# Kernel optimization log

Measured on AMD Instinct MI355X. Metric: run time of the kernel, lower is better.

## Reference

```python
import jax, jax.numpy as jnp
import numpy as np

N_HEADS = 16
ROPE_BASE = 10000.0

def apply_rope(x):
    # x: [B, H, S, D] with D even; interleaved-pair RoPE (torchtune style)
    B, H, S, D = x.shape
    half = D // 2
    inv_freq = 1.0 / (ROPE_BASE ** (jnp.arange(0, half, dtype=jnp.float32) / half))
    angles = jnp.arange(S, dtype=jnp.float32)[:, None] * inv_freq[None, :]  # [S, D/2]
    cos = jnp.cos(angles)[None, None]  # [1,1,S,D/2]
    sin = jnp.sin(angles)[None, None]
    x1 = x[..., 0::2]
    x2 = x[..., 1::2]
    r1 = x1 * cos - x2 * sin
    r2 = x1 * sin + x2 * cos
    return jnp.stack([r1, r2], axis=-1).reshape(B, H, S, D)

def setup_inputs() -> dict:
    key = jax.random.key(0)
    ks = jax.random.split(key, 5)
    B, S, E = 2, 2048, 1024
    d_attn = 1024
    scale = 1.0 / np.sqrt(E)
    x = jax.random.normal(ks[0], (B, S, E), dtype=jnp.float32)
    Wq = jax.random.normal(ks[1], (d_attn, E), dtype=jnp.float32) * scale
    Wk = jax.random.normal(ks[2], (d_attn, E), dtype=jnp.float32) * scale
    Wv = jax.random.normal(ks[3], (d_attn, E), dtype=jnp.float32) * scale
    Wo = jax.random.normal(ks[4], (E, d_attn), dtype=jnp.float32) * scale
    return {"x": x, "Wq": Wq, "Wk": Wk, "Wv": Wv, "Wo": Wo}

def reference(x, Wq, Wk, Wv, Wo):
    B, S, E = x.shape
    d_attn = Wq.shape[0]
    hd = d_attn // N_HEADS
    attn_scale = 1.0 / np.sqrt(d_attn)
    # projections (nn.Linear: x @ W.T), split heads -> [B, H, S, hd]
    q = (x @ Wq.T).reshape(B, S, N_HEADS, hd).transpose(0, 2, 1, 3)
    k = (x @ Wk.T).reshape(B, S, N_HEADS, hd).transpose(0, 2, 1, 3)
    v = (x @ Wv.T).reshape(B, S, N_HEADS, hd).transpose(0, 2, 1, 3)
    q = apply_rope(q)
    k = apply_rope(k)
    scores = jnp.einsum('bhqd,bhkd->bhqk', q, k) * attn_scale  # [B,H,S,S]
    causal = jnp.tril(jnp.ones((S, S), dtype=bool))
    scores = jnp.where(causal[None, None], scores, -jnp.inf)
    probs = jax.nn.softmax(scores, axis=-1)  # dropout is identity in eval
    out = jnp.einsum('bhqk,bhkd->bhqd', probs, v)
    out = out.transpose(0, 2, 1, 3).reshape(B, S, d_attn)
    return out @ Wo.T
```

## Files before the change

kernel.cpp:

```cpp
#include <hip/hip_runtime.h>


typedef float  f32x4  __attribute__((ext_vector_type(4)));
typedef short  short8 __attribute__((ext_vector_type(8)));

#define MFMA16(a,b,c) __builtin_amdgcn_mfma_f32_16x16x32_bf16((a),(b),(c),0,0,0)
#define GLD_LDS16(g, l)                                                        \
  __builtin_amdgcn_global_load_lds(                                            \
      (const __attribute__((address_space(1))) unsigned int*)(g),              \
      (__attribute__((address_space(3))) unsigned int*)(l), 16, 0, 0)

__device__ __forceinline__ unsigned short f2bf(float f) {
  unsigned int x = __float_as_uint(f);
  x += 0x7fffu + ((x >> 16) & 1u);
  return (unsigned short)(x >> 16);
}
__device__ __forceinline__ float bf2f(unsigned short u) {
  return __uint_as_float(((unsigned int)u) << 16);
}
__device__ __forceinline__ unsigned int cvtpk_bf16(float lo, float hi) {
  unsigned int r;
  asm("v_cvt_pk_bf16_f32 %0, %1, %2" : "=v"(r) : "v"(lo), "v"(hi));
  return r;
}

__global__ __launch_bounds__(256) void cvt_all(const float* __restrict__ x,
                                               const float* __restrict__ wq,
                                               const float* __restrict__ wk,
                                               const float* __restrict__ wv,
                                               const float* __restrict__ wo,
                                               ushort* __restrict__ dst) {
  const int i = blockIdx.x * 256 + threadIdx.x;
  const float* src;
  int off;
  if (i < 1048576) { src = x; off = i; }
  else {
    const int j = i - 1048576;
    const int wsel = j >> 18;
    off = j & 262143;
    src = (wsel == 0) ? wq : (wsel == 1) ? wk : (wsel == 2) ? wv : wo;
  }
  const float4 v = ((const float4*)src)[off];
  ushort4 o = make_ushort4(f2bf(v.x), f2bf(v.y), f2bf(v.z), f2bf(v.w));
  ((ushort4*)dst)[i] = o;
}

template<int MODE, int BN, int BM>
__global__ __launch_bounds__(256) void gemm_bt(const ushort* __restrict__ A,
                                               const ushort* __restrict__ B,
                                               void* __restrict__ Cv,
                                               int K) {
  constexpr int NI = BN / 32;
  constexpr int MI = BM / 32;
  constexpr int AI = BM / 64;
  constexpr int BI = BN / 64;
  __shared__ __align__(16) short As0[BM * 32];
  __shared__ __align__(16) short As1[BM * 32];
  __shared__ __align__(16) short Bs0[BN * 32];
  __shared__ __align__(16) short Bs1[BN * 32];
  const int tid  = threadIdx.x;
  const int lane = tid & 63, w = tid >> 6;
  const int ln   = lane & 15, quad = lane >> 4;
  const int wm   = w >> 1, wn = w & 1;
  const int m0 = blockIdx.y * BM, n0 = blockIdx.x * BN;

  const int srow = lane >> 2;
  const int schk = (lane & 3) * 8;
  const int arow = w * (16 * AI);
  const int brow = w * (16 * BI);
  const ushort* Ag0 = A + (size_t)(m0 + arow + srow) * K + schk;
  const ushort* Ag1 = A + (size_t)(m0 + arow + 16 + srow) * K + schk;
  const ushort* Bg0 = B + (size_t)(n0 + brow + srow) * K + schk;
  const ushort* Bg1 = B + (size_t)(n0 + brow + 16 + srow) * K + schk;
  const int lA0 = arow * 32, lA1 = (arow + 16) * 32;
  const int lB0 = brow * 32, lB1 = (brow + 16) * 32;

  int aoff[MI], boff[NI];
#pragma unroll
  for (int i = 0; i < MI; i++)
    aoff[i] = (wm * (BM / 2) + i * 16 + ln) * 32 + quad * 8;
#pragma unroll
  for (int i = 0; i < NI; i++)
    boff[i] = (wn * (BN / 2) + i * 16 + ln) * 32 + quad * 8;
  f32x4 acc[MI][NI] = {};

  for (int kt = 0; kt < K; kt += 64) {
    __syncthreads();
    GLD_LDS16(Ag0 + kt, As0 + lA0);
    if (AI == 2) GLD_LDS16(Ag1 + kt, As0 + lA1);
    GLD_LDS16(Ag0 + kt + 32, As1 + lA0);
    if (AI == 2) GLD_LDS16(Ag1 + kt + 32, As1 + lA1);
    GLD_LDS16(Bg0 + kt, Bs0 + lB0);
    if (BI == 2) GLD_LDS16(Bg1 + kt, Bs0 + lB1);
    GLD_LDS16(Bg0 + kt + 32, Bs1 + lB0);
    if (BI == 2) GLD_LDS16(Bg1 + kt + 32, Bs1 + lB1);
    __syncthreads();
#pragma unroll
    for (int h = 0; h < 2; ++h) {
      const short* Ap = h ? As1 : As0;
      const short* Bp = h ? Bs1 : Bs0;
      short8 av[MI], bv[NI];
#pragma unroll
      for (int i = 0; i < MI; i++) av[i] = *(const short8*)&Ap[aoff[i]];
#pragma unroll
      for (int i = 0; i < NI; i++) bv[i] = *(const short8*)&Bp[boff[i]];
#pragma unroll
      for (int mi = 0; mi < MI; mi++)
#pragma unroll
        for (int ni = 0; ni < NI; ni++)
          acc[mi][ni] = MFMA16(av[mi], bv[ni], acc[mi][ni]);
    }
  }

  if (MODE == 0) {
    ushort* Cq = (ushort*)Cv;
    if (n0 < 2048) {
      ushort* dst = Cq + (n0 < 1024 ? 0 : 4194304);
      const int nbase = (n0 < 1024) ? n0 : n0 - 1024;
      const float qsc = (n0 < 1024) ? 0.04508422002778011f : 1.0f;
      const float sgn = (ln & 1) ? 1.0f : -1.0f;
      float invc[NI];
#pragma unroll
      for (int ni = 0; ni < NI; ni++) {
        const int ii = ((wn * (BN / 2) + ni * 16 + ln) & 63) >> 1;
        invc[ni] = __builtin_amdgcn_exp2f(-(float)ii * 0.4152410118579865f) *
                   0.15915494309189535f;
      }
#pragma unroll
      for (int mi = 0; mi < MI; mi++) {
        const int row = m0 + wm * (BM / 2) + mi * 16 + quad * 4;
#pragma unroll
        for (int ni = 0; ni < NI; ni++) {
          const int col = nbase + wn * (BN / 2) + ni * 16 + ln;
#pragma unroll
          for (int r = 0; r < 4; r++) {
            const float mine  = acc[mi][ni][r];
            const float other = __shfl_xor(mine, 1, 64);
            const int   s     = (row + r) & 2047;
            const float rev   = (float)s * invc[ni];
            const float rr    = rev - floorf(rev);
            const float sn = __builtin_amdgcn_sinf(rr);
            const float cs = __builtin_amdgcn_cosf(rr);
            const float rot = (mine * cs + sgn * other * sn) * qsc;
            dst[(size_t)(row + r) * 1024 + col] = f2bf(rot);
          }
        }
      }
    } else {
      ushort* vt = Cq + 8388608;
#pragma unroll
      for (int mi = 0; mi < MI; mi++) {
        const int sm = m0 + wm * (BM / 2) + mi * 16 + quad * 4;
        const int b = sm >> 11, s = sm & 2047;
#pragma unroll
        for (int ni = 0; ni < NI; ni++) {
          const int nv = (n0 - 2048) + wn * (BN / 2) + ni * 16 + ln;
          const int bh = b * 16 + (nv >> 6), d = nv & 63;
          ushort4 u = make_ushort4(f2bf(acc[mi][ni][0]), f2bf(acc[mi][ni][1]),
                                   f2bf(acc[mi][ni][2]), f2bf(acc[mi][ni][3]));
          *(ushort4*)&vt[((size_t)bh * 64 + d) * 2048 + s] = u;
        }
      }
    }
  } else {
    float* C = (float*)Cv;
#pragma unroll
    for (int mi = 0; mi < MI; mi++) {
      const int row = m0 + wm * (BM / 2) + mi * 16 + quad * 4;
#pragma unroll
      for (int ni = 0; ni < NI; ni++) {
        const int col = n0 + wn * (BN / 2) + ni * 16 + ln;
#pragma unroll
        for (int r = 0; r < 4; r++)
          C[(size_t)(row + r) * 1024 + col] = acc[mi][ni][r];
      }
    }
  }
}

__global__ __launch_bounds__(512) void attnk(const ushort* __restrict__ q,
                                             const ushort* __restrict__ k,
                                             const ushort* __restrict__ vt,
                                             ushort* __restrict__ ctx) {
  __shared__ __align__(16) short Ks[2][64 * 72];
  __shared__ __align__(16) short Vs[2][64 * 72];
  __shared__ __align__(16) short Ps[8 * 16 * 72];
  const int tid  = threadIdx.x;
  const int lane = tid & 63, w = tid >> 6;
  const int ln   = lane & 15, quad = lane >> 4;
  const int x = blockIdx.x, bh = blockIdx.y;
  const int b = bh >> 4, h = bh & 15;
  const int jA = x, jB = 31 - x;
  const int tile = w >> 2;
  const int wq   = w & 3;
  const int j    = tile ? jA : jB;
  short* Pw = Ps + w * 1152;

  const size_t qb = ((size_t)(b * 2048 + j * 64 + wq * 16 + ln)) * 1024 + h * 64;
  const short8 aq0 = *(const short8*)&q[qb + quad * 8];
  const short8 aq1 = *(const short8*)&q[qb + 32 + quad * 8];

  f32x4 o[4] = {};
  float ls0 = 0.f, ls1 = 0.f;

  const int r0 = tid >> 3, c0 = (tid & 7) * 8;
  const ushort* kg = k  + ((size_t)(b * 2048 + r0)) * 1024 + h * 64 + c0;
  const ushort* vg = vt + ((size_t)(bh * 64 + r0)) * 2048 + c0;
  const int wK = r0 * 72 + c0;

  short8 kr = *(const short8*)(kg);
  short8 vr = *(const short8*)(vg);
  *(short8*)&Ks[0][wK] = kr;
  *(short8*)&Vs[0][wK] = vr;
  kr = *(const short8*)(kg + 65536);
  vr = *(const short8*)(vg + 64);

  const int qloc = j * 64 + wq * 16 + ln;

  for (int t = 0; t <= jB; t++) {
    __syncthreads();
    const short* Kc = Ks[t & 1];
    const short* Vc = Vs[t & 1];
    if (t < jB) {
      *(short8*)&Ks[(t & 1) ^ 1][wK] = kr;
      *(short8*)&Vs[(t & 1) ^ 1][wK] = vr;
    }
    if (t + 2 <= jB) {
      kr = *(const short8*)(kg + (size_t)(t + 2) * 65536);
      vr = *(const short8*)(vg + (t + 2) * 64);
    }

    const bool act = (tile == 0) || (t <= jA);
    if (act) {
      f32x4 sc[4];
      __builtin_amdgcn_s_setprio(1);
#pragma unroll
      for (int ct = 0; ct < 4; ct++) {
        const short8 bk0 = *(const short8*)&Kc[(ct * 16 + ln) * 72 + quad * 8];
        const short8 bk1 = *(const short8*)&Kc[(ct * 16 + ln) * 72 + 32 + quad * 8];
        f32x4 z = {0.f, 0.f, 0.f, 0.f};
        z = MFMA16(bk0, aq0, z);
        z = MFMA16(bk1, aq1, z);
        sc[ct] = z;
      }
      __builtin_amdgcn_s_setprio(0);
      if (t == j) {
#pragma unroll
        for (int ct = 0; ct < 4; ct++) {
          const int kvb = (t << 6) + ct * 16 + quad * 4;
#pragma unroll
          for (int r = 0; r < 4; r++)
            if (kvb + r > qloc) sc[ct][r] = -100000.0f;
        }
      }

      short8 bv0[4], bv1[4];
#pragma unroll
      for (int dt = 0; dt < 4; dt++) {
        bv0[dt] = *(const short8*)&Vc[(dt * 16 + ln) * 72 + quad * 8];
        bv1[dt] = *(const short8*)&Vc[(dt * 16 + ln) * 72 + 32 + quad * 8];
      }

#pragma unroll
      for (int ct = 0; ct < 4; ct++) {
        const float p0 = __builtin_amdgcn_exp2f(sc[ct][0]);
        const float p1 = __builtin_amdgcn_exp2f(sc[ct][1]);
        const float p2 = __builtin_amdgcn_exp2f(sc[ct][2]);
        const float p3 = __builtin_amdgcn_exp2f(sc[ct][3]);
        ls0 += p0 + p1;
        ls1 += p2 + p3;
        const uint2 u = make_uint2(cvtpk_bf16(p0, p1), cvtpk_bf16(p2, p3));
        *(uint2*)&Pw[ln * 72 + ct * 16 + quad * 4] = u;
      }
      const short8 ap0 = *(const short8*)&Pw[ln * 72 + quad * 8];
      const short8 ap1 = *(const short8*)&Pw[ln * 72 + 32 + quad * 8];
      __builtin_amdgcn_s_setprio(1);
#pragma unroll
      for (int dt = 0; dt < 4; dt++) {
        o[dt] = MFMA16(ap0, bv0[dt], o[dt]);
        o[dt] = MFMA16(ap1, bv1[dt], o[dt]);
      }
      __builtin_amdgcn_s_setprio(0);
    }
  }

  float l = ls0 + ls1;
  l += __shfl_xor(l, 16, 64);
  l += __shfl_xor(l, 32, 64);

#pragma unroll
  for (int r = 0; r < 4; r++) {
    const float inv = 1.0f / __shfl(l, quad * 4 + r, 64);
    const int row = j * 64 + wq * 16 + quad * 4 + r;
#pragma unroll
    for (int dt = 0; dt < 4; dt++) {
      ctx[((size_t)(b * 2048 + row)) * 1024 + h * 64 + dt * 16 + ln] =
          f2bf(o[dt][r] * inv);
    }
  }
}

extern "C" void kernel_launch(void* const* d_in, const int* in_sizes, int n_in,
                              void* d_out, int out_size, void* d_ws, size_t ws_size,
                              hipStream_t stream) {
  const float* x  = (const float*)d_in[0];
  const float* Wq = (const float*)d_in[1];
  const float* Wk = (const float*)d_in[2];
  const float* Wv = (const float*)d_in[3];
  const float* Wo = (const float*)d_in[4];
  float* out = (float*)d_out;
  char* ws = (char*)d_ws;

  ushort* xb  = (ushort*)(ws);
  ushort* wqb = (ushort*)(ws + (size_t)(8  << 20));
  ushort* qb  = (ushort*)(ws + (size_t)(16 << 20));
  ushort* kb  = (ushort*)(ws + (size_t)(24 << 20));
  ushort* vtb = (ushort*)(ws + (size_t)(32 << 20));
  ushort* ctx = (ushort*)(ws + (size_t)(40 << 20));

  cvt_all<<<8192, 256, 0, stream>>>(x, Wq, Wk, Wv, Wo, xb);
  gemm_bt<0, 64, 128><<<dim3(48, 32), 256, 0, stream>>>(xb, wqb, (void*)qb, 1024);
  attnk<<<dim3(16, 32), 512, 0, stream>>>(qb, kb, vtb, ctx);
  gemm_bt<2, 64, 64><<<dim3(16, 64), 256, 0, stream>>>(ctx, wqb + 3145728 , (void*)out, 1024);
}
```

Baseline: 174.2 us.

## Software-pipeline GEMM K loop with triple-buffered LDS and async prefetch

Replaces the load-then-compute K loop, which had two barriers per 64-wide step, with a triple-buffered pipeline over 32-wide K slices. The next slice's global-to-LDS loads are issued before computing the current one, using a partial vmcnt wait and a single barrier per step. The goal is to overlap global memory latency with MFMA work. In exchange it uses more LDS, which may lower occupancy, and it relies on hand-tuned waitcnt counts being correct.

```diff
diff --git a/kernel.cpp b/kernel.cpp
--- a/kernel.cpp
+++ b/kernel.cpp
@@ -54,10 +54,9 @@
   constexpr int MI = BM / 32;
   constexpr int AI = BM / 64;
   constexpr int BI = BN / 64;
-  __shared__ __align__(16) short As0[BM * 32];
-  __shared__ __align__(16) short As1[BM * 32];
-  __shared__ __align__(16) short Bs0[BN * 32];
-  __shared__ __align__(16) short Bs1[BN * 32];
+  constexpr int NDMA = AI + BI;
+  __shared__ __align__(16) short As[3][BM * 32];
+  __shared__ __align__(16) short Bs[3][BN * 32];
   const int tid  = threadIdx.x;
   const int lane = tid & 63, w = tid >> 6;
   const int ln   = lane & 15, quad = lane >> 4;
@@ -84,32 +83,40 @@
     boff[i] = (wn * (BN / 2) + i * 16 + ln) * 32 + quad * 8;
   f32x4 acc[MI][NI] = {};
 
-  for (int kt = 0; kt < K; kt += 64) {
-    __syncthreads();
-    GLD_LDS16(Ag0 + kt, As0 + lA0);
-    if (AI == 2) GLD_LDS16(Ag1 + kt, As0 + lA1);
-    GLD_LDS16(Ag0 + kt + 32, As1 + lA0);
-    if (AI == 2) GLD_LDS16(Ag1 + kt + 32, As1 + lA1);
-    GLD_LDS16(Bg0 + kt, Bs0 + lB0);
-    if (BI == 2) GLD_LDS16(Bg1 + kt, Bs0 + lB1);
-    GLD_LDS16(Bg0 + kt + 32, Bs1 + lB0);
-    if (BI == 2) GLD_LDS16(Bg1 + kt + 32, Bs1 + lB1);
-    __syncthreads();
-#pragma unroll
-    for (int h = 0; h < 2; ++h) {
-      const short* Ap = h ? As1 : As0;
-      const short* Bp = h ? Bs1 : Bs0;
-      short8 av[MI], bv[NI];
-#pragma unroll
-      for (int i = 0; i < MI; i++) av[i] = *(const short8*)&Ap[aoff[i]];
-#pragma unroll
-      for (int i = 0; i < NI; i++) bv[i] = *(const short8*)&Bp[boff[i]];
-#pragma unroll
-      for (int mi = 0; mi < MI; mi++)
-#pragma unroll
-        for (int ni = 0; ni < NI; ni++)
-          acc[mi][ni] = MFMA16(av[mi], bv[ni], acc[mi][ni]);
-    }
+  auto stage = [&](int buf, int kt) {
+    GLD_LDS16(Ag0 + kt, As[buf] + lA0);
+    if (AI == 2) GLD_LDS16(Ag1 + kt, As[buf] + lA1);
+    GLD_LDS16(Bg0 + kt, Bs[buf] + lB0);
+    if (BI == 2) GLD_LDS16(Bg1 + kt, Bs[buf] + lB1);
+  };
+
+  const int NS = K >> 5;
+  stage(0, 0);
+  int cur = 0, nxt = 1;
+  for (int s = 0; s < NS; ++s) {
+    if (s + 1 < NS) {
+      stage(nxt, (s + 1) << 5);
+      if constexpr (NDMA == 3) asm volatile("s_waitcnt vmcnt(3)" ::: "memory");
+      else                     asm volatile("s_waitcnt vmcnt(2)" ::: "memory");
+    } else {
+      asm volatile("s_waitcnt vmcnt(0)" ::: "memory");
+    }
+    __builtin_amdgcn_s_barrier();
+    __builtin_amdgcn_sched_barrier(0);
+    const short* Ap = As[cur];
+    const short* Bp = Bs[cur];
+    short8 av[MI], bv[NI];
+#pragma unroll
+    for (int i = 0; i < MI; i++) av[i] = *(const short8*)&Ap[aoff[i]];
+#pragma unroll
+    for (int i = 0; i < NI; i++) bv[i] = *(const short8*)&Bp[boff[i]];
+#pragma unroll
+    for (int mi = 0; mi < MI; mi++)
+#pragma unroll
+      for (int ni = 0; ni < NI; ni++)
+        acc[mi][ni] = MFMA16(av[mi], bv[ni], acc[mi][ni]);
+    cur = nxt;
+    nxt = (nxt == 2) ? 0 : nxt + 1;
   }
 
   if (MODE == 0) {
```

New measurement: 183.5 us. +5.3%, slower.
